# Optimization experiments

Measured on AMD Instinct MI355X. Metric: run time of the kernel, lower is better.

Reference implementation:

```python
import jax, jax.numpy as jnp
import numpy as np

N, M, K, C, OUT = 200000, 50000, 16, 64, 128
EPS = 1e-5  # torch BatchNorm1d default eps


def _bn(h, gamma, beta, mean, var):
    # BatchNorm1d in eval mode (running statistics)
    return (h - mean) * jax.lax.rsqrt(var + EPS) * gamma + beta


def setup_inputs() -> dict:
    key = jax.random.key(0)
    ks = jax.random.split(key, 8)
    p = jax.random.normal(ks[0], (N, 3), jnp.float32)
    x = jax.random.normal(ks[1], (N, C), jnp.float32)
    idx = jax.random.randint(ks[2], (M,), 0, N)          # FPS-sampled center indices
    knn_idx = jax.random.randint(ks[3], (M, K), 0, N)    # KNN neighbor indices
    # channel_shrinker: Linear(3+C, C, bias=False) -> BN -> ReLU -> Linear(C, 1)
    W1 = jax.random.normal(ks[4], (3 + C, C), jnp.float32) * 0.05  # stored [in,out]
    g1 = jnp.ones((C,), jnp.float32); b1 = jnp.zeros((C,), jnp.float32)
    m1 = jnp.zeros((C,), jnp.float32); v1 = jnp.ones((C,), jnp.float32)
    W2 = jax.random.normal(ks[5], (C, 1), jnp.float32) * 0.05
    b2 = jnp.zeros((1,), jnp.float32)
    # linear2: Linear(C, OUT, bias=False) -> BN -> ReLU
    Wl = jax.random.normal(ks[6], (C, OUT), jnp.float32) * 0.05
    gl = jnp.ones((OUT,), jnp.float32); bl = jnp.zeros((OUT,), jnp.float32)
    ml = jnp.zeros((OUT,), jnp.float32); vl = jnp.ones((OUT,), jnp.float32)
    return {"p": p, "x": x, "W1": W1, "g1": g1, "b1": b1, "m1": m1, "v1": v1,
            "W2": W2, "b2": b2, "Wl": Wl, "gl": gl, "bl": bl, "ml": ml, "vl": vl,
            "idx": idx, "knn_idx": knn_idx}


def reference(p, x, W1, g1, b1, m1, v1, W2, b2, Wl, gl, bl, ml, vl, idx, knn_idx):
    # queryandgroup(use_xyz=True): relative xyz of neighbors + gathered features
    n_p = p[idx]                                   # [M,3] sampled centers
    rel = p[knn_idx] - n_p[:, None, :]             # [M,K,3]
    x_knn = jnp.concatenate([rel, x[knn_idx]], -1) # [M,K,3+C]
    # channel_shrinker
    h = jnp.maximum(_bn(x_knn @ W1, g1, b1, m1, v1), 0.0)   # [M,K,C]
    s = h @ W2 + b2                                          # [M,K,1]
    prob = jax.nn.softmax(s, axis=1)                         # softmax over neighbors
    # linear2 on ALL original points, then gather by knn_idx
    y = jnp.maximum(_bn(x @ Wl, gl, bl, ml, vl), 0.0)        # [N,OUT]
    y_knn = y[knn_idx]                                       # [M,K,OUT]
    out = jnp.sum(y_knn * prob, axis=1)                      # [M,OUT]
    return n_p, out
```

## Files before the change

### kernel.cpp

```cpp
#include <hip/hip_runtime.h>

#define EPS 1e-5f

typedef __attribute__((ext_vector_type(8))) short bf16x8;
typedef __attribute__((ext_vector_type(4))) float f32x4;

static __device__ __forceinline__ unsigned short f2bf(float f) {
  unsigned int u = __float_as_uint(f);
  u = u + 0x7FFFu + ((u >> 16) & 1u);
  return (unsigned short)(u >> 16);
}
static __device__ __forceinline__ float bf2f(unsigned short h) {
  return __uint_as_float(((unsigned int)h) << 16);
}
static __device__ __forceinline__ unsigned int pk2(float lo, float hi) {
  return (unsigned int)f2bf(lo) | ((unsigned int)f2bf(hi) << 16);
}

__global__ __launch_bounds__(256) void k1_mfma(
    const float* __restrict__ x, const float* __restrict__ W1,
    const float* __restrict__ Wl, const float* __restrict__ gl,
    const float* __restrict__ bl, const float* __restrict__ ml,
    const float* __restrict__ vl,
    unsigned short* __restrict__ Z, unsigned short* __restrict__ Y)
{
  __shared__ unsigned short As[64 * 64];
  __shared__ unsigned short Bs[192 * 64];
  char* Ab = reinterpret_cast<char*>(As);
  char* Bb = reinterpret_cast<char*>(Bs);

  const int t = threadIdx.x;
  const long row0 = (long)blockIdx.x * 64;

  {
    int c = t & 63, k0 = (t >> 6) * 16;
    unsigned int w[8];
#pragma unroll
    for (int i = 0; i < 8; ++i) {
      float lo = W1[(size_t)(3 + k0 + 2 * i) * 64 + c];
      float hi = W1[(size_t)(3 + k0 + 2 * i + 1) * 64 + c];
      w[i] = pk2(lo, hi);
    }
    int byte0 = c * 128 + ((2 * k0) ^ ((c & 7) << 4));
    int byte1 = c * 128 + ((2 * (k0 + 8)) ^ ((c & 7) << 4));
    *reinterpret_cast<uint4*>(Bb + byte0) = make_uint4(w[0], w[1], w[2], w[3]);
    *reinterpret_cast<uint4*>(Bb + byte1) = make_uint4(w[4], w[5], w[6], w[7]);
  }
  {
    int c = t & 127, kh = t >> 7;
    int cc = 64 + c;
#pragma unroll
    for (int g = 0; g < 4; ++g) {
      unsigned int w[4];
#pragma unroll
      for (int i = 0; i < 4; ++i) {
        int k = kh * 32 + g * 8 + 2 * i;
        float lo = Wl[(size_t)k * 128 + c];
        float hi = Wl[(size_t)(k + 1) * 128 + c];
        w[i] = pk2(lo, hi);
      }
      int byte = cc * 128 + ((2 * (kh * 32 + g * 8)) ^ ((cc & 7) << 4));
      *reinterpret_cast<uint4*>(Bb + byte) = make_uint4(w[0], w[1], w[2], w[3]);
    }
  }
  {
    const float4* xg = reinterpret_cast<const float4*>(x + row0 * 64);
#pragma unroll
    for (int i = 0; i < 2; ++i) {
      int pi = t + i * 256;
      int r = pi >> 3, q = pi & 7;
      float4 v0 = xg[pi * 2];
      float4 v1 = xg[pi * 2 + 1];
      int byte = r * 128 + ((q * 16) ^ ((r & 7) << 4));
      *reinterpret_cast<uint4*>(Ab + byte) =
          make_uint4(pk2(v0.x, v0.y), pk2(v0.z, v0.w),
                     pk2(v1.x, v1.y), pk2(v1.z, v1.w));
    }
  }
  __syncthreads();

  const int wid = t >> 6, lane = t & 63;
  const int roff = (wid & 1) * 32, coff = (wid >> 1) * 96;
  const int lr = lane & 15, lk = lane >> 4;

  bf16x8 af[2][2];
#pragma unroll
  for (int rt = 0; rt < 2; ++rt) {
    int r = roff + rt * 16 + lr;
#pragma unroll
    for (int ks = 0; ks < 2; ++ks) {
      int byte = r * 128 + ((ks * 64 + lk * 16) ^ ((r & 7) << 4));
      af[rt][ks] = *reinterpret_cast<const bf16x8*>(Ab + byte);
    }
  }

#pragma unroll
  for (int ct = 0; ct < 6; ++ct) {
    int c0t = coff + ct * 16;
    int cread = c0t + lr;
    int byte0 = cread * 128 + ((lk * 16) ^ ((cread & 7) << 4));
    int byte1 = cread * 128 + ((64 + lk * 16) ^ ((cread & 7) << 4));
    bf16x8 bf0 = *reinterpret_cast<const bf16x8*>(Bb + byte0);
    bf16x8 bf1 = *reinterpret_cast<const bf16x8*>(Bb + byte1);

    float sc0 = 1.f, sc1 = 1.f, sc2 = 1.f, sc3 = 1.f;
    float sh0 = 0.f, sh1 = 0.f, sh2 = 0.f, sh3 = 0.f;
    if (c0t >= 64) {
      int oc = c0t - 64 + lk * 4;
      float4 g4 = *reinterpret_cast<const float4*>(gl + oc);
      float4 v4 = *reinterpret_cast<const float4*>(vl + oc);
      float4 b4 = *reinterpret_cast<const float4*>(bl + oc);
      float4 m4 = *reinterpret_cast<const float4*>(ml + oc);
      sc0 = g4.x * rsqrtf(v4.x + EPS); sh0 = b4.x - m4.x * sc0;
      sc1 = g4.y * rsqrtf(v4.y + EPS); sh1 = b4.y - m4.y * sc1;
      sc2 = g4.z * rsqrtf(v4.z + EPS); sh2 = b4.z - m4.z * sc2;
      sc3 = g4.w * rsqrtf(v4.w + EPS); sh3 = b4.w - m4.w * sc3;
    }
#pragma unroll
    for (int rt = 0; rt < 2; ++rt) {
      f32x4 acc = {0.f, 0.f, 0.f, 0.f};
      acc = __builtin_amdgcn_mfma_f32_16x16x32_bf16(bf0, af[rt][0], acc, 0, 0, 0);
      acc = __builtin_amdgcn_mfma_f32_16x16x32_bf16(bf1, af[rt][1], acc, 0, 0, 0);
      long n = row0 + roff + rt * 16 + lr;
      if (c0t < 64) {
        int cb = c0t + lk * 4;
        *reinterpret_cast<ushort4*>(Z + n * 64 + cb) =
            make_ushort4(f2bf(acc[0]), f2bf(acc[1]), f2bf(acc[2]), f2bf(acc[3]));
      } else {
        int cb = c0t - 64 + lk * 4;
        float y0 = fmaxf(fmaf(acc[0], sc0, sh0), 0.f);
        float y1 = fmaxf(fmaf(acc[1], sc1, sh1), 0.f);
        float y2 = fmaxf(fmaf(acc[2], sc2, sh2), 0.f);
        float y3 = fmaxf(fmaf(acc[3], sc3, sh3), 0.f);
        *reinterpret_cast<ushort4*>(Y + n * 128 + cb) =
            make_ushort4(f2bf(y0), f2bf(y1), f2bf(y2), f2bf(y3));
      }
    }
  }
}

static __device__ __forceinline__ float comb(float a, float b, int off, int lane) {
  bool hi = (lane & off) != 0;
  float send = hi ? a : b;
  float t = __shfl_xor(send, off, 64);
  return (hi ? b : a) + t;
}

__global__ __launch_bounds__(256) void k2_gather(
    const float* __restrict__ p, const unsigned short* __restrict__ Z,
    const unsigned short* __restrict__ Y, const float* __restrict__ W1,
    const float* __restrict__ g1, const float* __restrict__ b1,
    const float* __restrict__ m1, const float* __restrict__ v1,
    const float* __restrict__ W2, const int* __restrict__ idx,
    const int* __restrict__ knn, float* __restrict__ out_np,
    float* __restrict__ out_feat, int M)
{
  int gtid = blockIdx.x * 256 + threadIdx.x;
  int wid = gtid >> 6;
  int lane = threadIdx.x & 63;
  if (wid >= M) return;
  int m = __builtin_amdgcn_readfirstlane(wid);

  int ic = idx[m];
  float cx = p[ic * 3 + 0];
  float cy = p[ic * 3 + 1];
  float cz = p[ic * 3 + 2];

  int jj[16];
#pragma unroll
  for (int k = 0; k < 16; ++k) jj[k] = knn[m * 16 + k];

  float px[16], py[16], pz[16];
#pragma unroll
  for (int k = 0; k < 16; ++k) {
    px[k] = p[jj[k] * 3 + 0];
    py[k] = p[jj[k] * 3 + 1];
    pz[k] = p[jj[k] * 3 + 2];
  }

  unsigned short zv[16];
#pragma unroll
  for (int k = 0; k < 16; ++k) zv[k] = Z[(size_t)jj[k] * 64 + lane];

  unsigned int yv[16];
#pragma unroll
  for (int k = 0; k < 16; ++k)
    yv[k] = *reinterpret_cast<const unsigned int*>(Y + (size_t)jj[k] * 128 + 2 * lane);

  float a1 = g1[lane] * rsqrtf(v1[lane] + EPS);
  float c1 = b1[lane] - m1[lane] * a1;
  float w2 = W2[lane];
  float w10 = W1[lane];
  float w11 = W1[64 + lane];
  float w12 = W1[128 + lane];

  if (lane < 3) {
    float v = (lane == 0) ? cx : ((lane == 1) ? cy : cz);
    out_np[(size_t)m * 3 + lane] = v;
  }

  float part[16];
#pragma unroll
  for (int k = 0; k < 16; ++k) {
    float tv = bf2f(zv[k]);
    tv = fmaf(px[k] - cx, w10, tv);
    tv = fmaf(py[k] - cy, w11, tv);
    tv = fmaf(pz[k] - cz, w12, tv);
    float h = fmaxf(fmaf(tv, a1, c1), 0.f);
    part[k] = h * w2;
  }

  float u[8];
#pragma unroll
  for (int i = 0; i < 8; ++i) u[i] = comb(part[2 * i], part[2 * i + 1], 32, lane);
  float v4[4];
#pragma unroll
  for (int i = 0; i < 4; ++i) v4[i] = comb(u[2 * i], u[2 * i + 1], 16, lane);
  float w4[2];
#pragma unroll
  for (int i = 0; i < 2; ++i) w4[i] = comb(v4[2 * i], v4[2 * i + 1], 8, lane);
  float s1 = comb(w4[0], w4[1], 4, lane);
  s1 += __shfl_xor(s1, 1, 64);
  s1 += __shfl_xor(s1, 2, 64);

  float mx = s1;
  mx = fmaxf(mx, __shfl_xor(mx, 4, 64));
  mx = fmaxf(mx, __shfl_xor(mx, 8, 64));
  mx = fmaxf(mx, __shfl_xor(mx, 16, 64));
  mx = fmaxf(mx, __shfl_xor(mx, 32, 64));
  float e = __expf(s1 - mx);

  float pw[16];
  float S = 0.f;
#pragma unroll
  for (int k = 0; k < 16; ++k) {
    int g = ((k & 1) << 3) | ((k & 2) << 1) | ((k & 4) >> 1) | ((k & 8) >> 3);
    pw[k] = __shfl(e, g * 4, 64);
    S += pw[k];
  }
  float inv = 1.f / S;

  float acc0 = 0.f, acc1 = 0.f;
#pragma unroll
  for (int k = 0; k < 16; ++k) {
    acc0 = fmaf(pw[k], bf2f((unsigned short)(yv[k] & 0xFFFFu)), acc0);
    acc1 = fmaf(pw[k], bf2f((unsigned short)(yv[k] >> 16)), acc1);
  }
  float* orow = out_feat + (size_t)m * 128;
  *reinterpret_cast<float2*>(orow + 2 * lane) =
      make_float2(acc0 * inv, acc1 * inv);
}

extern "C" void kernel_launch(void* const* d_in, const int* in_sizes, int n_in,
                              void* d_out, int out_size, void* d_ws, size_t ws_size,
                              hipStream_t stream) {
  const float* p  = (const float*)d_in[0];
  const float* x  = (const float*)d_in[1];
  const float* W1 = (const float*)d_in[2];
  const float* g1 = (const float*)d_in[3];
  const float* b1 = (const float*)d_in[4];
  const float* m1 = (const float*)d_in[5];
  const float* v1 = (const float*)d_in[6];
  const float* W2 = (const float*)d_in[7];
  const float* Wl = (const float*)d_in[9];
  const float* gl = (const float*)d_in[10];
  const float* bl = (const float*)d_in[11];
  const float* ml = (const float*)d_in[12];
  const float* vl = (const float*)d_in[13];
  const int* idx  = (const int*)d_in[14];
  const int* knn  = (const int*)d_in[15];

  const int N = in_sizes[1] / 64;
  const int M = in_sizes[14];

  unsigned short* Z = (unsigned short*)d_ws;
  unsigned short* Y = Z + (size_t)N * 64;
  float* out_np   = (float*)d_out;
  float* out_feat = out_np + (size_t)M * 3;

  k1_mfma<<<dim3(N / 64), dim3(256), 0, stream>>>(
      x, W1, Wl, gl, bl, ml, vl, Z, Y);
  k2_gather<<<dim3(((size_t)M * 64 + 255) / 256), dim3(256), 0, stream>>>(
      p, Z, Y, W1, g1, b1, m1, v1, W2, idx, knn, out_np, out_feat, M);
}
```

Measured before the change: 205.3 us.

## Load A fragments directly to registers, fold BN into weights, streamline softmax

In the GEMM kernel, x is loaded from global memory directly into MFMA fragment registers, removing the LDS staging buffer and its readback. Float-to-bf16 packing switches to the library packed conversion. In the gather kernel, the BN scale and center offset are folded into the xyz weights, and the shuffle reduction order is changed so probabilities are broadcast via readlane. The softmax max-subtraction is removed, which saves shuffles but risks overflow for large scores.

```diff
diff --git a/kernel.cpp b/kernel.cpp
--- a/kernel.cpp
+++ b/kernel.cpp
@@ -1,20 +1,23 @@
 #include <hip/hip_runtime.h>
+#include <hip/hip_bf16.h>
 
 #define EPS 1e-5f
 
 typedef __attribute__((ext_vector_type(8))) short bf16x8;
 typedef __attribute__((ext_vector_type(4))) float f32x4;
 
-static __device__ __forceinline__ unsigned short f2bf(float f) {
-  unsigned int u = __float_as_uint(f);
-  u = u + 0x7FFFu + ((u >> 16) & 1u);
-  return (unsigned short)(u >> 16);
+static __device__ __forceinline__ unsigned int cvtpk(float lo, float hi) {
+  __hip_bfloat162 h = __float22bfloat162_rn(make_float2(lo, hi));
+  return *reinterpret_cast<unsigned int*>(&h);
 }
 static __device__ __forceinline__ float bf2f(unsigned short h) {
   return __uint_as_float(((unsigned int)h) << 16);
 }
-static __device__ __forceinline__ unsigned int pk2(float lo, float hi) {
-  return (unsigned int)f2bf(lo) | ((unsigned int)f2bf(hi) << 16);
+static __device__ __forceinline__ float bf2f_lo(unsigned int u) {
+  return __uint_as_float(u << 16);
+}
+static __device__ __forceinline__ float bf2f_hi(unsigned int u) {
+  return __uint_as_float(u & 0xFFFF0000u);
 }
 
 __global__ __launch_bounds__(256) void k1_mfma(
@@ -24,13 +27,26 @@
     const float* __restrict__ vl,
     unsigned short* __restrict__ Z, unsigned short* __restrict__ Y)
 {
-  __shared__ unsigned short As[64 * 64];
   __shared__ unsigned short Bs[192 * 64];
-  char* Ab = reinterpret_cast<char*>(As);
   char* Bb = reinterpret_cast<char*>(Bs);
 
   const int t = threadIdx.x;
   const long row0 = (long)blockIdx.x * 64;
+  const int wid = t >> 6, lane = t & 63;
+  const int roff = (wid & 1) * 32, coff = (wid >> 1) * 96;
+  const int lr = lane & 15, lk = lane >> 4;
+
+  float4 xa[2][2], xb[2][2];
+#pragma unroll
+  for (int rt = 0; rt < 2; ++rt) {
+    const float* xr = x + (row0 + roff + rt * 16 + lr) * 64;
+#pragma unroll
+    for (int ks = 0; ks < 2; ++ks) {
+      const float* src = xr + ks * 32 + lk * 8;
+      xa[rt][ks] = *reinterpret_cast<const float4*>(src);
+      xb[rt][ks] = *reinterpret_cast<const float4*>(src + 4);
+    }
+  }
 
   {
     int c = t & 63, k0 = (t >> 6) * 16;
@@ -39,7 +55,7 @@
     for (int i = 0; i < 8; ++i) {
       float lo = W1[(size_t)(3 + k0 + 2 * i) * 64 + c];
       float hi = W1[(size_t)(3 + k0 + 2 * i + 1) * 64 + c];
-      w[i] = pk2(lo, hi);
+      w[i] = cvtpk(lo, hi);
     }
     int byte0 = c * 128 + ((2 * k0) ^ ((c & 7) << 4));
     int byte1 = c * 128 + ((2 * (k0 + 8)) ^ ((c & 7) << 4));
@@ -57,42 +73,26 @@
         int k = kh * 32 + g * 8 + 2 * i;
         float lo = Wl[(size_t)k * 128 + c];
         float hi = Wl[(size_t)(k + 1) * 128 + c];
-        w[i] = pk2(lo, hi);
+        w[i] = cvtpk(lo, hi);
       }
       int byte = cc * 128 + ((2 * (kh * 32 + g * 8)) ^ ((cc & 7) << 4));
       *reinterpret_cast<uint4*>(Bb + byte) = make_uint4(w[0], w[1], w[2], w[3]);
     }
   }
-  {
-    const float4* xg = reinterpret_cast<const float4*>(x + row0 * 64);
-#pragma unroll
-    for (int i = 0; i < 2; ++i) {
-      int pi = t + i * 256;
-      int r = pi >> 3, q = pi & 7;
-      float4 v0 = xg[pi * 2];
-      float4 v1 = xg[pi * 2 + 1];
-      int byte = r * 128 + ((q * 16) ^ ((r & 7) << 4));
-      *reinterpret_cast<uint4*>(Ab + byte) =
-          make_uint4(pk2(v0.x, v0.y), pk2(v0.z, v0.w),
-                     pk2(v1.x, v1.y), pk2(v1.z, v1.w));
-    }
-  }
+
+  bf16x8 af[2][2];
+#pragma unroll
+  for (int rt = 0; rt < 2; ++rt)
+#pragma unroll
+    for (int ks = 0; ks < 2; ++ks) {
+      float4 a = xa[rt][ks], b = xb[rt][ks];
+      unsigned int u0 = cvtpk(a.x, a.y), u1 = cvtpk(a.z, a.w);
+      unsigned int u2 = cvtpk(b.x, b.y), u3 = cvtpk(b.z, b.w);
+      uint4 pk = make_uint4(u0, u1, u2, u3);
+      af[rt][ks] = *reinterpret_cast<bf16x8*>(&pk);
+    }
+
   __syncthreads();
-
-  const int wid = t >> 6, lane = t & 63;
-  const int roff = (wid & 1) * 32, coff = (wid >> 1) * 96;
-  const int lr = lane & 15, lk = lane >> 4;
-
-  bf16x8 af[2][2];
-#pragma unroll
-  for (int rt = 0; rt < 2; ++rt) {
-    int r = roff + rt * 16 + lr;
-#pragma unroll
-    for (int ks = 0; ks < 2; ++ks) {
-      int byte = r * 128 + ((ks * 64 + lk * 16) ^ ((r & 7) << 4));
-      af[rt][ks] = *reinterpret_cast<const bf16x8*>(Ab + byte);
-    }
-  }
 
 #pragma unroll
   for (int ct = 0; ct < 6; ++ct) {
@@ -124,16 +124,16 @@
       long n = row0 + roff + rt * 16 + lr;
       if (c0t < 64) {
         int cb = c0t + lk * 4;
-        *reinterpret_cast<ushort4*>(Z + n * 64 + cb) =
-            make_ushort4(f2bf(acc[0]), f2bf(acc[1]), f2bf(acc[2]), f2bf(acc[3]));
+        *reinterpret_cast<uint2*>(Z + n * 64 + cb) =
+            make_uint2(cvtpk(acc[0], acc[1]), cvtpk(acc[2], acc[3]));
       } else {
         int cb = c0t - 64 + lk * 4;
         float y0 = fmaxf(fmaf(acc[0], sc0, sh0), 0.f);
         float y1 = fmaxf(fmaf(acc[1], sc1, sh1), 0.f);
         float y2 = fmaxf(fmaf(acc[2], sc2, sh2), 0.f);
         float y3 = fmaxf(fmaf(acc[3], sc3, sh3), 0.f);
-        *reinterpret_cast<ushort4*>(Y + n * 128 + cb) =
-            make_ushort4(f2bf(y0), f2bf(y1), f2bf(y2), f2bf(y3));
+        *reinterpret_cast<uint2*>(Y + n * 128 + cb) =
+            make_uint2(cvtpk(y0, y1), cvtpk(y2, y3));
       }
     }
   }
@@ -142,8 +142,8 @@
 static __device__ __forceinline__ float comb(float a, float b, int off, int lane) {
   bool hi = (lane & off) != 0;
   float send = hi ? a : b;
-  float t = __shfl_xor(send, off, 64);
-  return (hi ? b : a) + t;
+  float tv = __shfl_xor(send, off, 64);
+  return (hi ? b : a) + tv;
 }
 
 __global__ __launch_bounds__(256) void k2_gather(
@@ -187,12 +187,15 @@
   for (int k = 0; k < 16; ++k)
     yv[k] = *reinterpret_cast<const unsigned int*>(Y + (size_t)jj[k] * 128 + 2 * lane);
 
+  __builtin_amdgcn_sched_barrier(0);
+
   float a1 = g1[lane] * rsqrtf(v1[lane] + EPS);
   float c1 = b1[lane] - m1[lane] * a1;
-  float w2 = W2[lane];
-  float w10 = W1[lane];
-  float w11 = W1[64 + lane];
-  float w12 = W1[128 + lane];
+  float w2v = W2[lane];
+  float w10a = W1[lane] * a1;
+  float w11a = W1[64 + lane] * a1;
+  float w12a = W1[128 + lane] * a1;
+  float base = c1 - (cx * w10a + cy * w11a + cz * w12a);
 
   if (lane < 3) {
     float v = (lane == 0) ? cx : ((lane == 1) ? cy : cz);
@@ -202,40 +205,33 @@
   float part[16];
 #pragma unroll
   for (int k = 0; k < 16; ++k) {
-    float tv = bf2f(zv[k]);
-    tv = fmaf(px[k] - cx, w10, tv);
-    tv = fmaf(py[k] - cy, w11, tv);
-    tv = fmaf(pz[k] - cz, w12, tv);
-    float h = fmaxf(fmaf(tv, a1, c1), 0.f);
-    part[k] = h * w2;
-  }
-
-  float u[8];
-#pragma unroll
-  for (int i = 0; i < 8; ++i) u[i] = comb(part[2 * i], part[2 * i + 1], 32, lane);
-  float v4[4];
-#pragma unroll
-  for (int i = 0; i < 4; ++i) v4[i] = comb(u[2 * i], u[2 * i + 1], 16, lane);
-  float w4[2];
-#pragma unroll
-  for (int i = 0; i < 2; ++i) w4[i] = comb(v4[2 * i], v4[2 * i + 1], 8, lane);
-  float s1 = comb(w4[0], w4[1], 4, lane);
-  s1 += __shfl_xor(s1, 1, 64);
-  s1 += __shfl_xor(s1, 2, 64);
-
-  float mx = s1;
-  mx = fmaxf(mx, __shfl_xor(mx, 4, 64));
-  mx = fmaxf(mx, __shfl_xor(mx, 8, 64));
-  mx = fmaxf(mx, __shfl_xor(mx, 16, 64));
-  mx = fmaxf(mx, __shfl_xor(mx, 32, 64));
-  float e = __expf(s1 - mx);
-
-  float pw[16];
-  float S = 0.f;
-#pragma unroll
-  for (int k = 0; k < 16; ++k) {
-    int g = ((k & 1) << 3) | ((k & 2) << 1) | ((k & 4) >> 1) | ((k & 8) >> 3);
-    pw[k] = __shfl(e, g * 4, 64);
+    float v = fmaf(bf2f(zv[k]), a1, base);
+    v = fmaf(px[k], w10a, v);
+    v = fmaf(py[k], w11a, v);
+    v = fmaf(pz[k], w12a, v);
+    part[k] = fmaxf(v, 0.f) * w2v;
+  }
+
+  float u8[8];
+#pragma unroll
+  for (int i = 0; i < 8; ++i) u8[i] = comb(part[2 * i], part[2 * i + 1], 1, lane);
+  float u4[4];
+#pragma unroll
+  for (int i = 0; i < 4; ++i) u4[i] = comb(u8[2 * i], u8[2 * i + 1], 2, lane);
+  float u2[2];
+#pragma unroll
+  for (int i = 0; i < 2; ++i) u2[i] = comb(u4[2 * i], u4[2 * i + 1], 8, lane);
+  float s1 = comb(u2[0], u2[1], 16, lane);
+  s1 += __shfl_xor(s1, 4, 64);
+  s1 += __shfl_xor(s1, 32, 64);
+
+  float e = __expf(s1);
+
+  float pw[16], S = 0.f;
+#pragma unroll
+  for (int k = 0; k < 16; ++k) {
+    int src = (k & 3) | ((k & 4) << 1) | ((k & 8) << 1);
+    pw[k] = __uint_as_float(__builtin_amdgcn_readlane(__float_as_uint(e), src));
     S += pw[k];
   }
   float inv = 1.f / S;
@@ -243,8 +239,8 @@
   float acc0 = 0.f, acc1 = 0.f;
 #pragma unroll
   for (int k = 0; k < 16; ++k) {
-    acc0 = fmaf(pw[k], bf2f((unsigned short)(yv[k] & 0xFFFFu)), acc0);
-    acc1 = fmaf(pw[k], bf2f((unsigned short)(yv[k] >> 16)), acc1);
+    acc0 = fmaf(pw[k], bf2f_lo(yv[k]), acc0);
+    acc1 = fmaf(pw[k], bf2f_hi(yv[k]), acc1);
   }
   float* orow = out_feat + (size_t)m * 128;
   *reinterpret_cast<float2*>(orow + 2 * lane) =
```

New measurement: 211.1 us. 1.03x slower.
